# Performance work log

Hardware: AMD Instinct MI355X
Metric: run time of the kernel (lower is better)

The kernel has to match this reference:

```python
import jax, jax.numpy as jnp
import numpy as np

N, E = 50000, 800000
NODE_DIM, EDGE_DIM, HIDDEN = 128, 32, 128


def setup_inputs() -> dict:
    key = jax.random.key(0)
    ks = jax.random.split(key, 12)
    def lin(k, fan_in, shape):
        bound = 1.0 / np.sqrt(fan_in)
        return jax.random.uniform(k, shape, jnp.float32, -bound, bound)
    return {
        "x": jax.random.normal(ks[0], (N, NODE_DIM), jnp.float32),
        "edge_index": jax.random.randint(ks[1], (2, E), 0, N),
        "edge_attr": jax.random.normal(ks[2], (E, EDGE_DIM), jnp.float32),
        # msg MLP: Linear(node+edge -> hidden), Linear(hidden -> hidden)
        "W1": lin(ks[3], NODE_DIM + EDGE_DIM, (HIDDEN, NODE_DIM + EDGE_DIM)),
        "b1": lin(ks[4], NODE_DIM + EDGE_DIM, (HIDDEN,)),
        "W2": lin(ks[5], HIDDEN, (HIDDEN, HIDDEN)),
        "b2": lin(ks[6], HIDDEN, (HIDDEN,)),
        # GRUCell(input=HIDDEN, hidden=NODE_DIM); gate order r,z,n (torch)
        "W_ih": lin(ks[7], NODE_DIM, (3 * NODE_DIM, HIDDEN)),
        "b_ih": lin(ks[8], NODE_DIM, (3 * NODE_DIM,)),
        "W_hh": lin(ks[9], NODE_DIM, (3 * NODE_DIM, NODE_DIM)),
        "b_hh": lin(ks[10], NODE_DIM, (3 * NODE_DIM,)),
    }


def reference(x, edge_index, edge_attr, W1, b1, W2, b2, W_ih, b_ih, W_hh, b_hh):
    src, dst = edge_index[0], edge_index[1]
    # gather + edge MLP: [E, node+edge] -> [E, hidden]
    m_in = jnp.concatenate([x[src], edge_attr], axis=-1)
    h1 = jax.nn.silu(m_in @ W1.T + b1)
    m = jax.nn.silu(h1 @ W2.T + b2)
    # scatter-add messages per destination node
    agg = jax.ops.segment_sum(m, dst, num_segments=x.shape[0])  # [N, hidden]
    # GRUCell: gates in torch order (r, z, n)
    gi = agg @ W_ih.T + b_ih  # [N, 3*node_dim]
    gh = x @ W_hh.T + b_hh
    i_r, i_z, i_n = jnp.split(gi, 3, axis=-1)
    h_r, h_z, h_n = jnp.split(gh, 3, axis=-1)
    r = jax.nn.sigmoid(i_r + h_r)
    z = jax.nn.sigmoid(i_z + h_z)
    n = jnp.tanh(i_n + r * h_n)
    return (1.0 - z) * n + z * x
```

## Files before the change

kernel.cpp:

```cpp
#include <hip/hip_runtime.h>
#include <hip/hip_bf16.h>
#include <cstdint>

typedef __bf16 bf16x8 __attribute__((ext_vector_type(8)));
typedef __bf16 bf16x4 __attribute__((ext_vector_type(4)));
typedef float  f32x4  __attribute__((ext_vector_type(4)));

#define ND 128
#define HID 128

__device__ __forceinline__ f32x4 mfma_bf16(bf16x8 a, bf16x8 b, f32x4 c) {
  return __builtin_amdgcn_mfma_f32_16x16x32_bf16(a, b, c, 0, 0, 0);
}
__device__ __forceinline__ float fast_sigmoid(float x) {
  return __fdividef(1.f, 1.f + __expf(-x));
}
__device__ __forceinline__ float fast_silu(float x) {
  return __fdividef(x, 1.f + __expf(-x));
}
__device__ __forceinline__ float fast_tanh(float x) {
  float cx = fminf(fmaxf(x, -15.f), 15.f);
  float e = __expf(2.f * cx);
  return __fdividef(e - 1.f, e + 1.f);
}

__global__ void k_prep(const float* __restrict__ s0, __bf16* __restrict__ d0, int c1,
                       const float* __restrict__ s1, __bf16* __restrict__ d1, int c2,
                       const float* __restrict__ s2, __bf16* __restrict__ d2, int c3,
                       const float* __restrict__ s3, __bf16* __restrict__ d3, int c4,
                       const float* __restrict__ s4, __bf16* __restrict__ d4, int c5,
                       float* __restrict__ agg, int aggz,
                       int* __restrict__ counts, int cntz) {
  int i = blockIdx.x * blockDim.x + threadIdx.x;
  if (i < c5) {
    const float* s; __bf16* d; int j;
    if (i < c1)      { s = s0; d = d0; j = i; }
    else if (i < c2) { s = s1; d = d1; j = i - c1; }
    else if (i < c3) { s = s2; d = d2; j = i - c2; }
    else if (i < c4) { s = s3; d = d3; j = i - c3; }
    else             { s = s4; d = d4; j = i - c4; }
    const float4* sp = reinterpret_cast<const float4*>(s) + (size_t)j * 2;
    float4 a = sp[0], b = sp[1];
    bf16x8 v;
    v[0] = (__bf16)a.x; v[1] = (__bf16)a.y; v[2] = (__bf16)a.z; v[3] = (__bf16)a.w;
    v[4] = (__bf16)b.x; v[5] = (__bf16)b.y; v[6] = (__bf16)b.z; v[7] = (__bf16)b.w;
    reinterpret_cast<bf16x8*>(d)[j] = v;
    return;
  }
  int k = i - c5;
  if (k < aggz) {
    float4 z = make_float4(0.f, 0.f, 0.f, 0.f);
    float4* p = reinterpret_cast<float4*>(agg) + (size_t)k * 2;
    p[0] = z; p[1] = z;
    return;
  }
  k -= aggz;
  if (k < cntz) {
    int4 z = make_int4(0, 0, 0, 0);
    int4* p = reinterpret_cast<int4*>(counts) + (size_t)k * 2;
    p[0] = z; p[1] = z;
  }
}

__global__ void k_hist(const int* __restrict__ dst, int* __restrict__ counts, int E) {
  int e = blockIdx.x * 256 + threadIdx.x;
  if (e < E) atomicAdd(&counts[dst[e]], 1);
}

__global__ void k_blocksum(const int* __restrict__ counts, int* __restrict__ bsum) {
  __shared__ int sd[256];
  int t = threadIdx.x;
  sd[t] = counts[blockIdx.x * 256 + t];
  __syncthreads();
  for (int d = 128; d > 0; d >>= 1) { if (t < d) sd[t] += sd[t + d]; __syncthreads(); }
  if (!t) bsum[blockIdx.x] = sd[0];
}

__global__ void k_scan_bsum(int* __restrict__ bsum, int nb) {
  __shared__ int sd[256];
  int t = threadIdx.x;
  int v = (t < nb) ? bsum[t] : 0;
  sd[t] = v;
  __syncthreads();
  for (int d = 1; d < 256; d <<= 1) {
    int u = (t >= d) ? sd[t - d] : 0;
    __syncthreads();
    sd[t] += u;
    __syncthreads();
  }
  if (t < nb) bsum[t] = sd[t] - v;
}

__global__ void k_scan_write(const int* __restrict__ counts, const int* __restrict__ bsum,
                             int* __restrict__ cursor) {
  __shared__ int sd[256];
  int t = threadIdx.x, b = blockIdx.x;
  int i = b * 256 + t;
  int c = counts[i];
  sd[t] = c;
  __syncthreads();
  for (int d = 1; d < 256; d <<= 1) {
    int u = (t >= d) ? sd[t - d] : 0;
    __syncthreads();
    sd[t] += u;
    __syncthreads();
  }
  cursor[i] = bsum[b] + sd[t] - c;
}

__global__ void k_perm(const int* __restrict__ src, const int* __restrict__ dst,
                       int* __restrict__ cursor, int4* __restrict__ einfo, int E) {
  int e = blockIdx.x * 256 + threadIdx.x;
  if (e < E) {
    int d = dst[e];
    int p = atomicAdd(&cursor[d], 1);
    einfo[p] = make_int4(src[e], d, e, 0);
  }
}

#define TILE_E 64

__global__ __launch_bounds__(512, 4) void edge_mlp8(
    const __bf16* __restrict__ xb,
    const float*  __restrict__ ea,
    const __bf16* __restrict__ W1b,
    const float*  __restrict__ b1,
    const __bf16* __restrict__ W2b,
    const float*  __restrict__ b2,
    const int4*   __restrict__ einfo,
    float* __restrict__ agg,
    int ntiles)
{
  __shared__ __bf16 Als[TILE_E * 160];
  __shared__ __bf16 H1[TILE_E * 128];
  __shared__ int dstls[TILE_E];
  char* AB = (char*)Als;
  char* HB = (char*)H1;

  const int tid = threadIdx.x;
  const int w  = tid >> 6;
  const int l  = tid & 63;
  const int l4 = l >> 4;
  const int lm = l & 15;
  const int jb = w * 16;

  bf16x8 bw1[5], bw2[4];
  {
    const int jr = jb + lm;
#pragma unroll
    for (int kt = 0; kt < 5; ++kt)
      bw1[kt] = *reinterpret_cast<const bf16x8*>(W1b + (size_t)jr * 160 + kt * 32 + l4 * 8);
#pragma unroll
    for (int kt = 0; kt < 4; ++kt)
      bw2[kt] = *reinterpret_cast<const bf16x8*>(W2b + (size_t)jr * 128 + kt * 32 + l4 * 8);
  }
  const float4 b1v = *reinterpret_cast<const float4*>(b1 + jb + l4 * 4);
  const float4 b2v = *reinterpret_cast<const float4*>(b2 + jb + l4 * 4);

  const int xslot = tid >> 4, xq = tid & 15;
  const int aslot = tid >> 3, aq = tid & 7;

  bf16x8 pxv0 = {}, pxv1 = {};
  float4 pea_ = {};
  int pdst_ = 0;

  auto PREFETCH = [&](int t) {
    int p0 = t * TILE_E;
    int s0 = einfo[p0 + xslot].x;
    int s1 = einfo[p0 + xslot + 32].x;
    pxv0 = *reinterpret_cast<const bf16x8*>(xb + (size_t)s0 * ND + xq * 8);
    pxv1 = *reinterpret_cast<const bf16x8*>(xb + (size_t)s1 * ND + xq * 8);
    int e2 = einfo[p0 + aslot].z;
    pea_ = reinterpret_cast<const float4*>(ea)[(size_t)e2 * 8 + aq];
    if (tid < TILE_E) pdst_ = einfo[p0 + tid].y;
  };

  int nwg = gridDim.x;
  int q = nwg >> 3, r = nwg & 7;
  int xcd = blockIdx.x & 7, pos = blockIdx.x >> 3;
  int swz = (xcd < r ? xcd * (q + 1) : r * (q + 1) + (xcd - r) * q) + pos;

  int tile = swz;
  if (tile < ntiles) PREFETCH(tile);

  for (; tile < ntiles; tile += gridDim.x) {
    __syncthreads();

    {
      int s_ = xslot;
      *reinterpret_cast<bf16x8*>(AB + s_ * 320 + ((xq ^ (s_ & 7)) << 4)) = pxv0;
      int s2 = xslot + 32;
      *reinterpret_cast<bf16x8*>(AB + s2 * 320 + ((xq ^ (s2 & 7)) << 4)) = pxv1;
    }
    {
      bf16x4 h;
      h[0] = (__bf16)pea_.x; h[1] = (__bf16)pea_.y;
      h[2] = (__bf16)pea_.z; h[3] = (__bf16)pea_.w;
      int pc = 16 + ((aq >> 1) ^ (aslot & 3));
      *reinterpret_cast<bf16x4*>(AB + aslot * 320 + (pc << 4) + ((aq & 1) << 3)) = h;
    }
    if (tid < TILE_E) dstls[tid] = pdst_;
    __syncthreads();

    int nt = tile + gridDim.x;
    if (nt < ntiles) PREFETCH(nt);

    __builtin_amdgcn_s_setprio(1);
#pragma unroll
    for (int et = 0; et < 4; ++et) {
      const int s_ = et * 16 + lm;
      const int sw = s_ & 7;
      f32x4 acc = {0.f, 0.f, 0.f, 0.f};
#pragma unroll
      for (int kt = 0; kt < 4; ++kt) {
        bf16x8 bfrag = *reinterpret_cast<const bf16x8*>(AB + s_ * 320 + (((kt * 4 + l4) ^ sw) << 4));
        acc = mfma_bf16(bw1[kt], bfrag, acc);
      }
      {
        bf16x8 bfrag = *reinterpret_cast<const bf16x8*>(AB + s_ * 320 + ((16 + (l4 ^ (s_ & 3))) << 4));
        acc = mfma_bf16(bw1[4], bfrag, acc);
      }
      bf16x4 h0;
#pragma unroll
      for (int rr = 0; rr < 4; ++rr)
        h0[rr] = (__bf16)fast_silu(acc[rr] + (&b1v.x)[rr]);
      int c0 = w * 2 + (l4 >> 1);
      int inner = (l4 & 1) << 3;
      *reinterpret_cast<bf16x4*>(HB + s_ * 256 + ((c0 ^ sw) << 4) + inner) = h0;
    }
    __syncthreads();

#pragma unroll
    for (int et = 0; et < 4; ++et) {
      const int s_ = et * 16 + lm;
      const int sw = s_ & 7;
      f32x4 acc = {0.f, 0.f, 0.f, 0.f};
#pragma unroll
      for (int kt = 0; kt < 4; ++kt) {
        bf16x8 bfrag = *reinterpret_cast<const bf16x8*>(HB + s_ * 256 + (((kt * 4 + l4) ^ sw) << 4));
        acc = mfma_bf16(bw2[kt], bfrag, acc);
      }
      bf16x4 m0;
#pragma unroll
      for (int rr = 0; rr < 4; ++rr)
        m0[rr] = (__bf16)fast_silu(acc[rr] + (&b2v.x)[rr]);
      int c0 = w * 2 + (l4 >> 1);
      int inner = (l4 & 1) << 3;
      *reinterpret_cast<bf16x4*>(AB + s_ * 256 + ((c0 ^ sw) << 4) + inner) = m0;
    }
    __builtin_amdgcn_s_setprio(0);
    __syncthreads();

    if (w < 4) {
      const int base = w * 16;
      int myd = dstls[base + (l & 15)];
      float a0 = 0.f, a1 = 0.f;
      int cur = __builtin_amdgcn_readlane(myd, 0);
#pragma unroll
      for (int i = 0; i < 16; ++i) {
        int nd = __builtin_amdgcn_readlane(myd, i);
        if (nd != cur) {
          atomicAdd(agg + (size_t)cur * HID + l * 2, a0);
          atomicAdd(agg + (size_t)cur * HID + l * 2 + 1, a1);
          a0 = 0.f; a1 = 0.f; cur = nd;
        }
        int ss = base + i;
        uint32_t u = *reinterpret_cast<const uint32_t*>(
            AB + ss * 256 + (((l >> 2) ^ (ss & 7)) << 4) + ((l & 3) << 2));
        a0 += __uint_as_float(u << 16);
        a1 += __uint_as_float(u & 0xffff0000u);
      }
      atomicAdd(agg + (size_t)cur * HID + l * 2, a0);
      atomicAdd(agg + (size_t)cur * HID + l * 2 + 1, a1);
    }
  }
}

__global__ __launch_bounds__(512) void gru3(
    const float*  __restrict__ agg,
    const __bf16* __restrict__ xb,
    const float*  __restrict__ x,
    const __bf16* __restrict__ Wih, const float* __restrict__ bih,
    const __bf16* __restrict__ Whh, const float* __restrict__ bhh,
    float* __restrict__ out, int N, int ntilesN)
{
  const int tid = threadIdx.x;
  const int w = tid >> 6, l = tid & 63;
  const int l4 = l >> 4, lm = l & 15;
  const int jb = w * 16;
  const int jr = jb + lm, jz = jr + 128, jn = jr + 256;

  bf16x8 WiR[4], WhR[4], WiZ[4], WhZ[4], WiN[4], WhN[4];
#pragma unroll
  for (int kt = 0; kt < 4; ++kt) {
    int ko = kt * 32 + l4 * 8;
    WiR[kt] = *reinterpret_cast<const bf16x8*>(Wih + (size_t)jr * ND + ko);
    WhR[kt] = *reinterpret_cast<const bf16x8*>(Whh + (size_t)jr * ND + ko);
    WiZ[kt] = *reinterpret_cast<const bf16x8*>(Wih + (size_t)jz * ND + ko);
    WhZ[kt] = *reinterpret_cast<const bf16x8*>(Whh + (size_t)jz * ND + ko);
    WiN[kt] = *reinterpret_cast<const bf16x8*>(Wih + (size_t)jn * ND + ko);
    WhN[kt] = *reinterpret_cast<const bf16x8*>(Whh + (size_t)jn * ND + ko);
  }
  float4 birv, bizv, binv, bhnv;
  {
    int j0 = jb + l4 * 4;
    float4 a = *reinterpret_cast<const float4*>(bih + j0);
    float4 b = *reinterpret_cast<const float4*>(bhh + j0);
    birv = make_float4(a.x + b.x, a.y + b.y, a.z + b.z, a.w + b.w);
    a = *reinterpret_cast<const float4*>(bih + 128 + j0);
    b = *reinterpret_cast<const float4*>(bhh + 128 + j0);
    bizv = make_float4(a.x + b.x, a.y + b.y, a.z + b.z, a.w + b.w);
    binv = *reinterpret_cast<const float4*>(bih + 256 + j0);
    bhnv = *reinterpret_cast<const float4*>(bhh + 256 + j0);
  }

  for (int bt = blockIdx.x; bt < ntilesN; bt += gridDim.x) {
    const int n0 = bt * 64;
#pragma unroll
    for (int rt = 0; rt < 4; ++rt) {
      const int node = n0 + rt * 16 + lm;
      const bool ok = node < N;
      bf16x8 aA[4], aX[4];
#pragma unroll
      for (int kt = 0; kt < 4; ++kt) {
        int ko = kt * 32 + l4 * 8;
        bf16x8 z8 = {};
        if (ok) {
          float4 a0 = *reinterpret_cast<const float4*>(agg + (size_t)node * ND + ko);
          float4 a1 = *reinterpret_cast<const float4*>(agg + (size_t)node * ND + ko + 4);
          bf16x8 v;
          v[0] = (__bf16)a0.x; v[1] = (__bf16)a0.y; v[2] = (__bf16)a0.z; v[3] = (__bf16)a0.w;
          v[4] = (__bf16)a1.x; v[5] = (__bf16)a1.y; v[6] = (__bf16)a1.z; v[7] = (__bf16)a1.w;
          aA[kt] = v;
          aX[kt] = *reinterpret_cast<const bf16x8*>(xb + (size_t)node * ND + ko);
        } else {
          aA[kt] = z8;
          aX[kt] = z8;
        }
      }
      f32x4 aR = {0.f,0.f,0.f,0.f}, aZ = {0.f,0.f,0.f,0.f};
      f32x4 ai = {0.f,0.f,0.f,0.f}, ah = {0.f,0.f,0.f,0.f};
#pragma unroll
      for (int kt = 0; kt < 4; ++kt) {
        aR = mfma_bf16(WiR[kt], aA[kt], aR);
        aR = mfma_bf16(WhR[kt], aX[kt], aR);
        aZ = mfma_bf16(WiZ[kt], aA[kt], aZ);
        aZ = mfma_bf16(WhZ[kt], aX[kt], aZ);
        ai = mfma_bf16(WiN[kt], aA[kt], ai);
        ah = mfma_bf16(WhN[kt], aX[kt], ah);
      }
      if (ok) {
        float4 xv = *reinterpret_cast<const float4*>(x + (size_t)node * ND + jb + l4 * 4);
        float4 ov;
#pragma unroll
        for (int rr = 0; rr < 4; ++rr) {
          float r = fast_sigmoid(aR[rr] + (&birv.x)[rr]);
          float z = fast_sigmoid(aZ[rr] + (&bizv.x)[rr]);
          float n = fast_tanh(ai[rr] + (&binv.x)[rr] + r * (ah[rr] + (&bhnv.x)[rr]));
          (&ov.x)[rr] = (1.f - z) * n + z * (&xv.x)[rr];
        }
        *reinterpret_cast<float4*>(out + (size_t)node * ND + jb + l4 * 4) = ov;
      }
    }
  }
}

extern "C" void kernel_launch(void* const* d_in, const int* in_sizes, int n_in,
                              void* d_out, int out_size, void* d_ws, size_t ws_size,
                              hipStream_t stream) {
  const float* x   = (const float*)d_in[0];
  const int*   ei  = (const int*)d_in[1];
  const float* ea  = (const float*)d_in[2];
  const float* W1  = (const float*)d_in[3];
  const float* b1  = (const float*)d_in[4];
  const float* W2  = (const float*)d_in[5];
  const float* b2  = (const float*)d_in[6];
  const float* Wih = (const float*)d_in[7];
  const float* bih = (const float*)d_in[8];
  const float* Whh = (const float*)d_in[9];
  const float* bhh = (const float*)d_in[10];
  float* out = (float*)d_out;
  const int N = in_sizes[0] / ND;
  const int E = in_sizes[1] / 2;

  const int nb = (N + 255) / 256;
  const int nC = nb * 256;

  char* ws = (char*)d_ws;
  size_t off = 0;
  auto alloc = [&](size_t bytes) -> void* {
    void* p = ws + off;
    off += (bytes + 255) & ~(size_t)255;
    return p;
  };
  __bf16* xb      = (__bf16*)alloc((size_t)N * ND * 2);
  __bf16* W1b     = (__bf16*)alloc(128 * 160 * 2);
  __bf16* W2b     = (__bf16*)alloc(128 * 128 * 2);
  __bf16* Wihb    = (__bf16*)alloc(384 * 128 * 2);
  __bf16* Whhb    = (__bf16*)alloc(384 * 128 * 2);
  int*    counts  = (int*)alloc((size_t)nC * 4);
  int*    cursor  = (int*)alloc((size_t)nC * 4);
  int*    bsum    = (int*)alloc(256 * 4);
  int4*   einfo   = (int4*)alloc((size_t)E * 16);
  float*  agg     = (float*)alloc((size_t)N * ND * 4);
  (void)ws_size;

  const int* srcp = ei;
  const int* dstp = ei + E;

  const int n8_x = N * ND / 8, n8_1 = 128 * 160 / 8, n8_2 = 128 * 128 / 8, n8_g = 384 * 128 / 8;
  int c1 = n8_x, c2 = c1 + n8_1, c3 = c2 + n8_2, c4 = c3 + n8_g, c5 = c4 + n8_g;
  int aggz = N * ND / 8;
  int cntz = nC / 8;
  int prep_total = c5 + aggz + cntz;
  k_prep<<<(prep_total + 255) / 256, 256, 0, stream>>>(
      x, xb, c1, W1, W1b, c2, W2, W2b, c3, Wih, Wihb, c4, Whh, Whhb, c5,
      agg, aggz, counts, cntz);

  k_hist<<<(E + 255) / 256, 256, 0, stream>>>(dstp, counts, E);
  k_blocksum<<<nb, 256, 0, stream>>>(counts, bsum);
  k_scan_bsum<<<1, 256, 0, stream>>>(bsum, nb);
  k_scan_write<<<nb, 256, 0, stream>>>(counts, bsum, cursor);
  k_perm<<<(E + 255) / 256, 256, 0, stream>>>(srcp, dstp, cursor, einfo, E);

  const int ntiles = E / TILE_E;
  edge_mlp8<<<2500, 512, 0, stream>>>(xb, ea, W1b, b1, W2b, b2,
                                      einfo, agg, ntiles);

  const int ntilesN = (N + 63) / 64;
  gru3<<<256, 512, 0, stream>>>(agg, xb, x, Wihb, bih, Whhb, bhh, out, N, ntilesN);
}
```

Before: 339.5 us.

## Use 1024-thread edge MLP blocks, merge scan kernels, size GRU grid to tiles

The edge MLP block grows to 16 waves, so each pair of waves shares the same weight columns and handles half of the 64-edge tile each. Gathers and the segmented atomic reduction are split across twice as many threads. The separate block-sum scan kernel is folded into the scan-write kernel, with each block rescanning the block sums itself. The GRU launch now uses one block per 64-node tile instead of 256 persistent blocks. Together these aim to raise parallelism and cut launch count, at the cost of more register pressure per block, more atomics from shorter segments, and redundant scan work.

```diff
diff --git a/kernel.cpp b/kernel.cpp
--- a/kernel.cpp
+++ b/kernel.cpp
@@ -76,9 +76,10 @@
   if (!t) bsum[blockIdx.x] = sd[0];
 }
 
-__global__ void k_scan_bsum(int* __restrict__ bsum, int nb) {
+__global__ void k_scan_write(const int* __restrict__ counts, const int* __restrict__ bsum,
+                             int* __restrict__ cursor, int nb) {
   __shared__ int sd[256];
-  int t = threadIdx.x;
+  int t = threadIdx.x, b = blockIdx.x;
   int v = (t < nb) ? bsum[t] : 0;
   sd[t] = v;
   __syncthreads();
@@ -88,13 +89,8 @@
     sd[t] += u;
     __syncthreads();
   }
-  if (t < nb) bsum[t] = sd[t] - v;
-}
-
-__global__ void k_scan_write(const int* __restrict__ counts, const int* __restrict__ bsum,
-                             int* __restrict__ cursor) {
-  __shared__ int sd[256];
-  int t = threadIdx.x, b = blockIdx.x;
+  int bexcl = (b == 0) ? 0 : sd[b - 1];
+  __syncthreads();
   int i = b * 256 + t;
   int c = counts[i];
   sd[t] = c;
@@ -105,7 +101,7 @@
     sd[t] += u;
     __syncthreads();
   }
-  cursor[i] = bsum[b] + sd[t] - c;
+  cursor[i] = bexcl + sd[t] - c;
 }
 
 __global__ void k_perm(const int* __restrict__ src, const int* __restrict__ dst,
@@ -120,7 +116,7 @@
 
 #define TILE_E 64
 
-__global__ __launch_bounds__(512, 4) void edge_mlp8(
+__global__ __launch_bounds__(1024, 2) void edge_mlp9(
     const __bf16* __restrict__ xb,
     const float*  __restrict__ ea,
     const __bf16* __restrict__ W1b,
@@ -142,7 +138,8 @@
   const int l  = tid & 63;
   const int l4 = l >> 4;
   const int lm = l & 15;
-  const int jb = w * 16;
+  const int jb = (w & 7) * 16;
+  const int sh = (w >> 3) * 32;
 
   bf16x8 bw1[5], bw2[4];
   {
@@ -160,18 +157,18 @@
   const int xslot = tid >> 4, xq = tid & 15;
   const int aslot = tid >> 3, aq = tid & 7;
 
-  bf16x8 pxv0 = {}, pxv1 = {};
+  bf16x8 pxv0 = {};
   float4 pea_ = {};
   int pdst_ = 0;
 
   auto PREFETCH = [&](int t) {
     int p0 = t * TILE_E;
     int s0 = einfo[p0 + xslot].x;
-    int s1 = einfo[p0 + xslot + 32].x;
     pxv0 = *reinterpret_cast<const bf16x8*>(xb + (size_t)s0 * ND + xq * 8);
-    pxv1 = *reinterpret_cast<const bf16x8*>(xb + (size_t)s1 * ND + xq * 8);
-    int e2 = einfo[p0 + aslot].z;
-    pea_ = reinterpret_cast<const float4*>(ea)[(size_t)e2 * 8 + aq];
+    if (tid < 512) {
+      int e2 = einfo[p0 + aslot].z;
+      pea_ = reinterpret_cast<const float4*>(ea)[(size_t)e2 * 8 + aq];
+    }
     if (tid < TILE_E) pdst_ = einfo[p0 + tid].y;
   };
 
@@ -186,13 +183,8 @@
   for (; tile < ntiles; tile += gridDim.x) {
     __syncthreads();
 
-    {
-      int s_ = xslot;
-      *reinterpret_cast<bf16x8*>(AB + s_ * 320 + ((xq ^ (s_ & 7)) << 4)) = pxv0;
-      int s2 = xslot + 32;
-      *reinterpret_cast<bf16x8*>(AB + s2 * 320 + ((xq ^ (s2 & 7)) << 4)) = pxv1;
-    }
-    {
+    *reinterpret_cast<bf16x8*>(AB + xslot * 320 + ((xq ^ (xslot & 7)) << 4)) = pxv0;
+    if (tid < 512) {
       bf16x4 h;
       h[0] = (__bf16)pea_.x; h[1] = (__bf16)pea_.y;
       h[2] = (__bf16)pea_.z; h[3] = (__bf16)pea_.w;
@@ -207,8 +199,8 @@
 
     __builtin_amdgcn_s_setprio(1);
 #pragma unroll
-    for (int et = 0; et < 4; ++et) {
-      const int s_ = et * 16 + lm;
+    for (int et = 0; et < 2; ++et) {
+      const int s_ = sh + et * 16 + lm;
       const int sw = s_ & 7;
       f32x4 acc = {0.f, 0.f, 0.f, 0.f};
 #pragma unroll
@@ -224,15 +216,15 @@
 #pragma unroll
       for (int rr = 0; rr < 4; ++rr)
         h0[rr] = (__bf16)fast_silu(acc[rr] + (&b1v.x)[rr]);
-      int c0 = w * 2 + (l4 >> 1);
+      int c0 = (w & 7) * 2 + (l4 >> 1);
       int inner = (l4 & 1) << 3;
       *reinterpret_cast<bf16x4*>(HB + s_ * 256 + ((c0 ^ sw) << 4) + inner) = h0;
     }
     __syncthreads();
 
 #pragma unroll
-    for (int et = 0; et < 4; ++et) {
-      const int s_ = et * 16 + lm;
+    for (int et = 0; et < 2; ++et) {
+      const int s_ = sh + et * 16 + lm;
       const int sw = s_ & 7;
       f32x4 acc = {0.f, 0.f, 0.f, 0.f};
 #pragma unroll
@@ -244,20 +236,20 @@
 #pragma unroll
       for (int rr = 0; rr < 4; ++rr)
         m0[rr] = (__bf16)fast_silu(acc[rr] + (&b2v.x)[rr]);
-      int c0 = w * 2 + (l4 >> 1);
+      int c0 = (w & 7) * 2 + (l4 >> 1);
       int inner = (l4 & 1) << 3;
       *reinterpret_cast<bf16x4*>(AB + s_ * 256 + ((c0 ^ sw) << 4) + inner) = m0;
     }
     __builtin_amdgcn_s_setprio(0);
     __syncthreads();
 
-    if (w < 4) {
-      const int base = w * 16;
-      int myd = dstls[base + (l & 15)];
+    if (w < 8) {
+      const int base = w * 8;
+      int myd = dstls[base + (l & 7)];
       float a0 = 0.f, a1 = 0.f;
       int cur = __builtin_amdgcn_readlane(myd, 0);
 #pragma unroll
-      for (int i = 0; i < 16; ++i) {
+      for (int i = 0; i < 8; ++i) {
         int nd = __builtin_amdgcn_readlane(myd, i);
         if (nd != cur) {
           atomicAdd(agg + (size_t)cur * HID + l * 2, a0);
@@ -419,14 +411,13 @@
 
   k_hist<<<(E + 255) / 256, 256, 0, stream>>>(dstp, counts, E);
   k_blocksum<<<nb, 256, 0, stream>>>(counts, bsum);
-  k_scan_bsum<<<1, 256, 0, stream>>>(bsum, nb);
-  k_scan_write<<<nb, 256, 0, stream>>>(counts, bsum, cursor);
+  k_scan_write<<<nb, 256, 0, stream>>>(counts, bsum, cursor, nb);
   k_perm<<<(E + 255) / 256, 256, 0, stream>>>(srcp, dstp, cursor, einfo, E);
 
   const int ntiles = E / TILE_E;
-  edge_mlp8<<<2500, 512, 0, stream>>>(xb, ea, W1b, b1, W2b, b2,
-                                      einfo, agg, ntiles);
+  edge_mlp9<<<1250, 1024, 0, stream>>>(xb, ea, W1b, b1, W2b, b2,
+                                       einfo, agg, ntiles);
 
   const int ntilesN = (N + 63) / 64;
-  gru3<<<256, 512, 0, stream>>>(agg, xb, x, Wihb, bih, Whhb, bhh, out, N, ntilesN);
-}
+  gru3<<<ntilesN, 512, 0, stream>>>(agg, xb, x, Wihb, bih, Whhb, bhh, out, N, ntilesN);
+}
```

New measurement: 405.3 us. 1.19x slower.
